# Optimization experiments

Measured on AMD Instinct MI355X. Metric: run time of the kernel, lower is better.

Reference implementation:

```python
import jax, jax.numpy as jnp
import numpy as np


def ste_sign(w):
    # straight-through binarization: forward sign(w), backward identity
    return w + jax.lax.stop_gradient(jnp.sign(w) - w)


def spike(x):
    # Heaviside spike with straight-through estimator
    return x + jax.lax.stop_gradient((x > 0).astype(x.dtype) - x)


def quantized_conv1d(x, w, b, stride, padding):
    # XNOR-Net style 1-bit weights: sign(w) * per-out-channel mean(|w|)
    alpha = jnp.mean(jnp.abs(w), axis=(1, 2), keepdims=True)  # (O,1,1)
    wq = ste_sign(w) * alpha
    y = jax.lax.conv_general_dilated(
        x, wq, window_strides=(stride,), padding=[(padding, padding)],
        dimension_numbers=('NCH', 'OIH', 'NCH'))
    return y + b[None, :, None]


def batchnorm(x, gamma, beta, eps=1e-5):
    # training-mode BN over (batch, length) per channel
    mu = jnp.mean(x, axis=(0, 2), keepdims=True)
    var = jnp.var(x, axis=(0, 2), keepdims=True)
    return (x - mu) * jax.lax.rsqrt(var + eps) * gamma[None, :, None] + beta[None, :, None]


def window_attn(sq, sk, sv, w):
    # spiking attention restricted to non-overlapping windows of size w
    B, L, C = sq.shape
    pad = (-L) % w
    p = lambda a: jnp.pad(a, ((0, 0), (0, pad), (0, 0)))  # zero-pad -> zero spikes
    q = p(sq).reshape(B, -1, w, C)
    k = p(sk).reshape(B, -1, w, C)
    v = p(sv).reshape(B, -1, w, C)
    attn = jnp.einsum('bnwc,bnuc->bnwu', q, k)           # (B, nW, w, w)
    out = jnp.einsum('bnwu,bnuc->bnwc', attn, v) / w
    return out.reshape(B, -1, C)[:, :L]


def global_attn(sq, K, V, g):
    # pool K,V down to g global tokens, then linear spiking attention
    B, L, C = K.shape
    chunk = -(-L // g)
    pad = chunk * g - L
    p = lambda a: jnp.pad(a, ((0, 0), (0, pad), (0, 0)))
    kp = p(K).reshape(B, g, chunk, C).mean(axis=2)       # (B, g, C)
    vp = p(V).reshape(B, g, chunk, C).mean(axis=2)
    skg, svg = spike(kp), spike(vp)
    kv = jnp.einsum('bgc,bgd->bcd', skg, svg)            # (B, C, C)
    return jnp.einsum('blc,bcd->bld', sq, kv) / g


def mssa(x, wq, wk, wv, wo, local_w=64, regional_w=256, global_pool=16):
    # x: (B, C, L) -> token-major (B, L, C)
    h = jnp.swapaxes(x, 1, 2)
    Q, K, V = h @ wq, h @ wk, h @ wv
    sq, sk, sv = spike(Q), spike(K), spike(V)
    out = (window_attn(sq, sk, sv, local_w)
           + window_attn(sq, sk, sv, regional_w)
           + global_attn(sq, K, V, global_pool)) / 3.0
    y = h + out @ wo  # residual
    return jnp.swapaxes(y, 1, 2)


def setup_inputs() -> dict:
    key = jax.random.key(0)
    ks = jax.random.split(key, 8)
    B, Cin, L, Cout = 32, 256, 5000, 128
    return {
        'x': jax.random.normal(ks[0], (B, Cin, L), jnp.float32),
        'conv_w': jax.random.normal(ks[1], (Cout, Cin, 9), jnp.float32) * 0.05,
        'conv_b': jnp.zeros((Cout,), jnp.float32),
        'gamma': jnp.ones((Cout,), jnp.float32),
        'beta': jnp.zeros((Cout,), jnp.float32),
        'wq': jax.random.normal(ks[2], (Cout, Cout), jnp.float32) * 0.09,
        'wk': jax.random.normal(ks[3], (Cout, Cout), jnp.float32) * 0.09,
        'wv': jax.random.normal(ks[4], (Cout, Cout), jnp.float32) * 0.09,
        'wo': jax.random.normal(ks[5], (Cout, Cout), jnp.float32) * 0.09,
    }


def reference(x, conv_w, conv_b, gamma, beta, wq, wk, wv, wo):
    y = quantized_conv1d(x, conv_w, conv_b, stride=2, padding=4)  # (B,128,2500)
    y = jax.nn.elu(batchnorm(y, gamma, beta))
    return mssa(y, wq, wk, wv, wo)                                # (B,128,2500)
```

## Files before the change

kernel.cpp:

```cpp
#include <hip/hip_runtime.h>

typedef __attribute__((ext_vector_type(8))) short bf16x8;
typedef __attribute__((ext_vector_type(4))) float f32x4;
typedef __attribute__((ext_vector_type(16))) float f32x16;
typedef __attribute__((ext_vector_type(4))) unsigned int u32x4;
typedef __attribute__((ext_vector_type(4))) int s32x4;
typedef unsigned short u16;
typedef unsigned int u32;

#define DI __device__ __forceinline__

constexpr int B_ = 32, CI = 256, LX = 5000, CO = 128, LO = 2500, KW = 9, LP = 2560;

DI float b2f(u16 u) { u32 x = ((u32)u) << 16; return __builtin_bit_cast(float, x); }
DI u16 f2b(float f) {
  u32 x = __builtin_bit_cast(u32, f);
  u32 r = (x + 0x7fffu + ((x >> 16) & 1u)) >> 16;
  return (u16)r;
}
DI float elu(float v) { return v > 0.f ? v : expm1f(v); }

__global__ __launch_bounds__(256) void k_prep_wq(const float* __restrict__ w, u16* __restrict__ wfmt,
                                                 float* __restrict__ alphaf) {
  int o = blockIdx.x;
  const float* wrow = w + o * CI * KW;
  float s = 0.f;
  for (int idx = threadIdx.x; idx < CI * KW; idx += 256) s += fabsf(wrow[idx]);
  __shared__ float red[256];
  red[threadIdx.x] = s;
  __syncthreads();
  for (int st = 128; st > 0; st >>= 1) {
    if (threadIdx.x < st) red[threadIdx.x] += red[threadIdx.x + st];
    __syncthreads();
  }
  if (threadIdx.x == 0) alphaf[o] = red[0] / (float)(CI * KW);
  for (int idx = threadIdx.x; idx < CI * KW; idx += 256) {
    int i = idx / KW, k = idx - i * KW;
    float v = wrow[idx];
    float sg = v > 0.f ? 1.f : (v < 0.f ? -1.f : 0.f);
    wfmt[(((k * 16) + (i >> 4)) * 128 + o) * 16 + (i & 15)] = f2b(sg);
  }
}

__global__ __launch_bounds__(256) void k_prep_wT(const float* __restrict__ wq, const float* __restrict__ wk,
                                                 const float* __restrict__ wv, const float* __restrict__ wo,
                                                 u16* __restrict__ wThi, u16* __restrict__ wTlo,
                                                 u16* __restrict__ wT3) {
  const float* src[4] = {wq, wk, wv, wo};
  int mat = blockIdx.x;
  const float* m = src[mat];
  u16* dh = wThi + mat * CO * CO;
  u16* dl = wTlo + mat * CO * CO;
  for (int idx = threadIdx.x; idx < CO * CO; idx += 256) {
    int nn = idx >> 7, kkn = idx & 127;
    float v = m[kkn * CO + nn];
    u16 hi = f2b(v);
    u16 lo = f2b(v - b2f(hi));
    dh[idx] = hi;
    dl[idx] = lo;
    if (mat < 3) {
      int nt = nn >> 4, n = nn & 15, ks = kkn >> 5, gj = kkn & 31;
      size_t base = (size_t)((mat * 4 + ks) * 8 + nt) * 1024 + n * 32 + gj;
      wT3[base] = hi;
      wT3[base + 512] = lo;
    }
  }
}

__global__ __launch_bounds__(512) void k_conv(const float* __restrict__ x, const u16* __restrict__ wfmt,
                                              const float* __restrict__ bias, const float* __restrict__ alphaf,
                                              float* __restrict__ y1) {
  const int ltile = blockIdx.x, b = blockIdx.y;
  const int l0 = ltile * 64;
  const int lin0 = 2 * l0 - 4;
  alignas(16) __shared__ u16 xsh[136 * 136];
  alignas(16) __shared__ u16 xsl[136 * 136];
  const int tid = threadIdx.x;
  const int wave = tid >> 6, lane = tid & 63;
  const int col = lane & 31, g = lane >> 5;
  const int o0 = (wave & 3) * 32;
  const int lw = (wave >> 2) * 32;
  f32x16 acch = {};
  f32x16 accl = {};
  for (int cpass = 0; cpass < 2; ++cpass) {
    const int c0 = cpass * 128;
    if (cpass) __syncthreads();
#pragma unroll
    for (int it = 0; it < 9; ++it) {
      int idx = tid + it * 512;
      if (idx < 4352) {
        int i = idx / 34, q = idx - i * 34;
        int lin = lin0 + q * 4;
        const float* xr = x + ((size_t)(b * CI + c0 + i)) * LX;
        float4 v4 = float4{0.f, 0.f, 0.f, 0.f};
        if (lin >= 0 && lin + 4 <= LX) v4 = *reinterpret_cast<const float4*>(xr + lin);
        const float* vp = reinterpret_cast<const float*>(&v4);
#pragma unroll
        for (int e = 0; e < 4; ++e) {
          int p = q * 4 + e;
          float v = vp[e];
          u16 hi = f2b(v);
          int colx = ((((i >> 3) ^ ((p >> 1) & 15)) & 15) << 3) | (i & 7);
          xsh[p * 136 + colx] = hi;
          xsl[p * 136 + colx] = f2b(v - b2f(hi));
        }
      }
    }
    __syncthreads();
    for (int kk = 0; kk < KW; ++kk) {
      bf16x8 af[8];
#pragma unroll
      for (int icg = 0; icg < 8; ++icg) {
        int chunk = kk * 16 + cpass * 8 + icg;
        af[icg] = *reinterpret_cast<const bf16x8*>(wfmt + ((size_t)chunk * 128 + o0 + col) * 16 + g * 8);
      }
      const int p = 2 * (lw + col) + kk;
      const int prow = p * 136;
      const int s = (p >> 1) & 15;
#pragma unroll
      for (int icg = 0; icg < 8; ++icg) {
        int blkoff = (((icg * 2 + g) ^ s) << 3);
        bf16x8 bh = *reinterpret_cast<const bf16x8*>(&xsh[prow + blkoff]);
        bf16x8 bl = *reinterpret_cast<const bf16x8*>(&xsl[prow + blkoff]);
        acch = __builtin_amdgcn_mfma_f32_32x32x16_bf16(af[icg], bh, acch, 0, 0, 0);
        accl = __builtin_amdgcn_mfma_f32_32x32x16_bf16(af[icg], bl, accl, 0, 0, 0);
      }
    }
  }
  const int l = l0 + lw + col;
  if (l < LO) {
#pragma unroll
    for (int r = 0; r < 16; ++r) {
      int o = o0 + (r & 3) + 8 * (r >> 2) + 4 * g;
      y1[(b * CO + o) * LO + l] = alphaf[o] * (acch[r] + accl[r]) + bias[o];
    }
  }
}

__global__ __launch_bounds__(256) void k_stats(const float* __restrict__ y1, float* __restrict__ ps,
                                               float* __restrict__ ps2) {
  int o = blockIdx.x, b = blockIdx.y;
  const float4* row = reinterpret_cast<const float4*>(y1 + (size_t)(b * CO + o) * LO);
  float s = 0.f, s2 = 0.f;
  for (int i = threadIdx.x; i < 625; i += 256) {
    float4 v = row[i];
    s += v.x + v.y + v.z + v.w;
    s2 += v.x * v.x + v.y * v.y + v.z * v.z + v.w * v.w;
  }
  __shared__ float r1[256], r2[256];
  r1[threadIdx.x] = s;
  r2[threadIdx.x] = s2;
  __syncthreads();
  for (int st = 128; st > 0; st >>= 1) {
    if (threadIdx.x < st) {
      r1[threadIdx.x] += r1[threadIdx.x + st];
      r2[threadIdx.x] += r2[threadIdx.x + st];
    }
    __syncthreads();
  }
  if (threadIdx.x == 0) {
    ps[b * CO + o] = r1[0];
    ps2[b * CO + o] = r2[0];
  }
}

__global__ void k_bnparams(const float* __restrict__ ps, const float* __restrict__ ps2,
                           const float* __restrict__ gamma, const float* __restrict__ beta,
                           float* __restrict__ bnsc, float* __restrict__ bnsh) {
  int o = threadIdx.x;
  float s = 0.f, s2 = 0.f;
  for (int b = 0; b < B_; ++b) {
    s += ps[b * CO + o];
    s2 += ps2[b * CO + o];
  }
  const float inv_n = 1.f / (float)(B_ * LO);
  float mu = s * inv_n;
  float var = s2 * inv_n - mu * mu;
  float sc = gamma[o] * rsqrtf(var + 1e-5f);
  bnsc[o] = sc;
  bnsh[o] = beta[o] - mu * sc;
}

__global__ __launch_bounds__(256) void k_qkv(const float* __restrict__ y1, const float* __restrict__ bnsc,
                                             const float* __restrict__ bnsh, const u16* __restrict__ wT3,
                                             signed char* __restrict__ sq8, signed char* __restrict__ sk8,
                                             u16* __restrict__ sv) {
  int tile = blockIdx.x, b = blockIdx.y;
  int tid = threadIdx.x, wave = tid >> 6, lane = tid & 63, n = lane & 15, g = lane >> 4;
  const int t0 = tile * 64;
  alignas(16) __shared__ u16 hshi[64 * 136];
  alignas(16) __shared__ u16 hslo[64 * 136];
  {
    int t = tid & 63;
    int l = t0 + t;
    if (l > LO - 1) l = LO - 1;
    for (int c = (tid >> 6); c < CO; c += 4) {
      float raw = y1[((size_t)b * CO + c) * LO + l];
      float e = elu(raw * bnsc[c] + bnsh[c]);
      u16 hi = f2b(e);
      hshi[t * 136 + c] = hi;
      hslo[t * 136 + c] = f2b(e - b2f(hi));
    }
  }
  __syncthreads();
  const u16* ah = &hshi[(wave * 16 + n) * 136];
  const u16* al = &hslo[(wave * 16 + n) * 136];
  for (int mat = 0; mat < 3; ++mat) {
    f32x4 acc[8] = {};
#pragma unroll
    for (int ks = 0; ks < 4; ++ks) {
      bf16x8 ahi = *reinterpret_cast<const bf16x8*>(ah + ks * 32 + g * 8);
      bf16x8 alo = *reinterpret_cast<const bf16x8*>(al + ks * 32 + g * 8);
      const u16* wbase = wT3 + (size_t)((mat * 4 + ks) * 8) * 1024 + n * 32 + g * 8;
#pragma unroll
      for (int nt = 0; nt < 8; ++nt) {
        bf16x8 bhi = *reinterpret_cast<const bf16x8*>(wbase + nt * 1024);
        bf16x8 blo = *reinterpret_cast<const bf16x8*>(wbase + nt * 1024 + 512);
        acc[nt] = __builtin_amdgcn_mfma_f32_16x16x32_bf16(ahi, bhi, acc[nt], 0, 0, 0);
        acc[nt] = __builtin_amdgcn_mfma_f32_16x16x32_bf16(ahi, blo, acc[nt], 0, 0, 0);
        acc[nt] = __builtin_amdgcn_mfma_f32_16x16x32_bf16(alo, bhi, acc[nt], 0, 0, 0);
        acc[nt] = __builtin_amdgcn_mfma_f32_16x16x32_bf16(alo, blo, acc[nt], 0, 0, 0);
      }
    }
#pragma unroll
    for (int nt = 0; nt < 8; ++nt) {
#pragma unroll
      for (int r = 0; r < 4; ++r) {
        int tok = t0 + wave * 16 + g * 4 + r;
        int c = nt * 16 + n;
        bool valid = tok < LO;
        float v = valid ? acc[nt][r] : 0.f;
        size_t oidx = ((size_t)b * LP + tok) * CO + c;
        if (mat == 2) {
          sv[oidx] = f2b(v > 0.f ? 1.f : 0.f);
        } else {
          signed char* so8 = (mat == 0) ? sq8 : sk8;
          so8[oidx] = v > 0.f ? 1 : 0;
        }
      }
    }
  }
}

__global__ __launch_bounds__(64) void k_poolh(const float* __restrict__ y1, const float* __restrict__ bnsc,
                                              const float* __restrict__ bnsh, float* __restrict__ hsum) {
  int c = blockIdx.x, b = blockIdx.y, lane = threadIdx.x;
  const float* row = y1 + ((size_t)b * CO + c) * LO;
  const float sc = bnsc[c], sh = bnsh[c];
  __shared__ float bins[16][64];
#pragma unroll
  for (int ch = 0; ch < 16; ++ch) bins[ch][lane] = 0.f;
  for (int j = lane; j < LO; j += 64) {
    float e = elu(row[j] * sc + sh);
    bins[j / 157][lane] += e;
  }
#pragma unroll
  for (int ch = 0; ch < 16; ++ch) {
    float v = bins[ch][lane];
    for (int off = 32; off > 0; off >>= 1) v += __shfl_down(v, off);
    if (lane == 0) hsum[(b * 16 + ch) * CO + c] = v;
  }
}

__global__ __launch_bounds__(256) void k_kv2(const float* __restrict__ hsum, const float* __restrict__ wk,
                                             const float* __restrict__ wv, signed char* __restrict__ kv8) {
  int b = blockIdx.x;
  __shared__ float hs[16 * 128], sks[16 * 128], svs[16 * 128];
  for (int i = threadIdx.x; i < 2048; i += 256) hs[i] = hsum[b * 2048 + i];
  __syncthreads();
  for (int idx = threadIdx.x; idx < 2048; idx += 256) {
    int gg = idx >> 7, c = idx & 127;
    float ak = 0.f, av = 0.f;
    for (int k = 0; k < 128; ++k) {
      float hv = hs[gg * 128 + k];
      ak += hv * wk[k * CO + c];
      av += hv * wv[k * CO + c];
    }
    sks[idx] = ak > 0.f ? 1.f : 0.f;
    svs[idx] = av > 0.f ? 1.f : 0.f;
  }
  __syncthreads();
  for (int idx = threadIdx.x; idx < CO * CO; idx += 256) {
    int d = idx >> 7, c = idx & 127;
    float s = 0.f;
#pragma unroll
    for (int gg = 0; gg < 16; ++gg) s += sks[gg * 128 + c] * svs[gg * 128 + d];
    kv8[b * CO * CO + idx] = (signed char)s;
  }
}

__global__ __launch_bounds__(512) void k_attn(const signed char* __restrict__ sq8,
                                              const signed char* __restrict__ sk8,
                                              const u16* __restrict__ sv, const signed char* __restrict__ kv8,
                                              const u16* __restrict__ woT, const float* __restrict__ y1,
                                              const float* __restrict__ bnsc, const float* __restrict__ bnsh,
                                              float* __restrict__ out) {
  const int win = blockIdx.x, b = blockIdx.y, qt = blockIdx.z;
  const int T0 = win * 256;
  alignas(16) __shared__ char smem[69632];
  u16* svT = reinterpret_cast<u16*>(smem);
  const int tid = threadIdx.x, wave = tid >> 6, lane = tid & 63, n = lane & 15, g = lane >> 4;
  for (int idx = tid; idx < 256 * 128; idx += 512) {
    int u = idx >> 7, c = idx & 127;
    svT[c * 264 + u] = sv[((size_t)b * LP + T0 + u) * CO + c];
  }
  __syncthreads();
  {
    const int qbase = wave * 32 + qt * 16;
    s32x4 bq8[2];
    const signed char* qrow = sq8 + ((size_t)b * LP + T0 + qbase + n) * CO;
    bq8[0] = *reinterpret_cast<const s32x4*>(qrow + g * 16);
    bq8[1] = *reinterpret_cast<const s32x4*>(qrow + 64 + g * 16);
    s32x4 pacc[16];
#pragma unroll
    for (int ut = 0; ut < 16; ++ut) pacc[ut] = s32x4{0, 0, 0, 0};
    for (int ut = 0; ut < 16; ++ut) {
      const signed char* krow = sk8 + ((size_t)b * LP + T0 + ut * 16 + n) * CO;
      s32x4 kf0 = *reinterpret_cast<const s32x4*>(krow + g * 16);
      s32x4 kf1 = *reinterpret_cast<const s32x4*>(krow + 64 + g * 16);
      pacc[ut] = __builtin_amdgcn_mfma_i32_16x16x64_i8(kf0, bq8[0], pacc[ut], 0, 0, 0);
      pacc[ut] = __builtin_amdgcn_mfma_i32_16x16x64_i8(kf1, bq8[1], pacc[ut], 0, 0, 0);
    }
    const int qblk = (qbase + n) >> 6;
    u32 packed[16][2];
#pragma unroll
    for (int ut = 0; ut < 16; ++ut) {
      u16 pk[4];
#pragma unroll
      for (int r = 0; r < 4; ++r) {
        int uloc = ut * 16 + g * 4 + r;
        float wgt = (1.f / 768.f) + (((uloc >> 6) == qblk) ? (1.f / 192.f) : 0.f);
        pk[r] = f2b((float)pacc[ut][r] * wgt);
      }
      packed[ut][0] = (u32)pk[0] | ((u32)pk[1] << 16);
      packed[ut][1] = (u32)pk[2] | ((u32)pk[3] << 16);
    }
    f32x4 acco[8];
#pragma unroll
    for (int ct = 0; ct < 8; ++ct) {
      s32x4 ag = {0, 0, 0, 0};
      const signed char* kvrow = kv8 + ((size_t)b * CO + ct * 16 + n) * CO;
      s32x4 k0 = *reinterpret_cast<const s32x4*>(kvrow + g * 16);
      s32x4 k1 = *reinterpret_cast<const s32x4*>(kvrow + 64 + g * 16);
      ag = __builtin_amdgcn_mfma_i32_16x16x64_i8(bq8[0], k0, ag, 0, 0, 0);
      ag = __builtin_amdgcn_mfma_i32_16x16x64_i8(bq8[1], k1, ag, 0, 0, 0);
#pragma unroll
      for (int r = 0; r < 4; ++r) acco[ct][r] = (float)ag[r] * (1.f / 48.f);
    }
    const int sl0 = n + 16 * ((g & 1) * 2);
    const int sl1 = sl0 + 16;
    const bool ghi = ((g >> 1) & 1) != 0;
#pragma unroll
    for (int us = 0; us < 8; ++us) {
      u32 a0e = (u32)__shfl((int)packed[us * 2][0], sl0, 64);
      u32 a0o = (u32)__shfl((int)packed[us * 2 + 1][0], sl0, 64);
      u32 a1e = (u32)__shfl((int)packed[us * 2][1], sl0, 64);
      u32 a1o = (u32)__shfl((int)packed[us * 2 + 1][1], sl0, 64);
      u32 a2e = (u32)__shfl((int)packed[us * 2][0], sl1, 64);
      u32 a2o = (u32)__shfl((int)packed[us * 2 + 1][0], sl1, 64);
      u32 a3e = (u32)__shfl((int)packed[us * 2][1], sl1, 64);
      u32 a3o = (u32)__shfl((int)packed[us * 2 + 1][1], sl1, 64);
      u32x4 paw = {ghi ? a0o : a0e, ghi ? a1o : a1e, ghi ? a2o : a2e, ghi ? a3o : a3e};
      bf16x8 pa = __builtin_bit_cast(bf16x8, paw);
#pragma unroll
      for (int ct = 0; ct < 8; ++ct) {
        bf16x8 bv = *reinterpret_cast<const bf16x8*>(&svT[(ct * 16 + n) * 264 + us * 32 + g * 8]);
        acco[ct] = __builtin_amdgcn_mfma_f32_16x16x32_bf16(pa, bv, acco[ct], 0, 0, 0);
      }
    }
    __syncthreads();
    u16* pw2 = reinterpret_cast<u16*>(smem) + wave * (16 * 136);
    float* sF = reinterpret_cast<float*>(smem + 34816) + wave * (64 * 17);
#pragma unroll
    for (int ct = 0; ct < 8; ++ct) {
#pragma unroll
      for (int r = 0; r < 4; ++r) {
        pw2[(g * 4 + r) * 136 + ct * 16 + n] = f2b(acco[ct][r]);
      }
    }
    for (int half = 0; half < 2; ++half) {
#pragma unroll
      for (int ot2 = 0; ot2 < 4; ++ot2) {
        int ot = half * 4 + ot2;
        f32x4 facc = {};
#pragma unroll
        for (int ks = 0; ks < 4; ++ks) {
          bf16x8 af = *reinterpret_cast<const bf16x8*>(&pw2[n * 136 + ks * 32 + g * 8]);
          bf16x8 bw = *reinterpret_cast<const bf16x8*>(woT + (ot * 16 + n) * CO + ks * 32 + g * 8);
          facc = __builtin_amdgcn_mfma_f32_16x16x32_bf16(af, bw, facc, 0, 0, 0);
        }
#pragma unroll
        for (int r = 0; r < 4; ++r) sF[(ot2 * 16 + n) * 17 + g * 4 + r] = facc[r];
      }
#pragma unroll
      for (int oo = 0; oo < 16; ++oo) {
        int olocal = oo * 4 + (lane >> 4);
        int o = half * 64 + olocal;
        int l = T0 + qbase + (lane & 15);
        float v = sF[olocal * 17 + (lane & 15)];
        if (l < LO) {
          size_t idx = ((size_t)b * CO + o) * LO + l;
          out[idx] = elu(y1[idx] * bnsc[o] + bnsh[o]) + v;
        }
      }
    }
  }
}

extern "C" void kernel_launch(void* const* d_in, const int* in_sizes, int n_in, void* d_out, int out_size,
                              void* d_ws, size_t ws_size, hipStream_t stream) {
  const float* x = (const float*)d_in[0];
  const float* conv_w = (const float*)d_in[1];
  const float* conv_b = (const float*)d_in[2];
  const float* gamma = (const float*)d_in[3];
  const float* beta = (const float*)d_in[4];
  const float* wq = (const float*)d_in[5];
  const float* wk = (const float*)d_in[6];
  const float* wv = (const float*)d_in[7];
  const float* wo = (const float*)d_in[8];
  (void)in_sizes; (void)n_in; (void)out_size; (void)ws_size;

  char* ws = (char*)d_ws;
  size_t off = 0;
  auto alloc = [&](size_t bytes) -> void* {
    void* p = ws + off;
    off += (bytes + 511) & ~(size_t)511;
    return p;
  };
  float* ps = (float*)alloc((size_t)B_ * CO * 4);
  float* ps2 = (float*)alloc((size_t)B_ * CO * 4);
  float* bnsc = (float*)alloc(CO * 4);
  float* bnsh = (float*)alloc(CO * 4);
  float* alphaf = (float*)alloc(CO * 4);
  float* hsum = (float*)alloc((size_t)B_ * 16 * CO * 4);
  signed char* kv8 = (signed char*)alloc((size_t)B_ * CO * CO);
  u16* wfmt = (u16*)alloc((size_t)CO * KW * CI * 2);
  u16* wThi = (u16*)alloc((size_t)4 * CO * CO * 2);
  u16* wTlo = (u16*)alloc((size_t)4 * CO * CO * 2);
  u16* wT3 = (u16*)alloc((size_t)3 * 4 * 8 * 1024 * 2);
  float* y1 = (float*)alloc((size_t)B_ * CO * LO * 4);
  signed char* sqb8 = (signed char*)alloc((size_t)B_ * LP * CO);
  signed char* skb8 = (signed char*)alloc((size_t)B_ * LP * CO);
  u16* svb = (u16*)alloc((size_t)B_ * LP * CO * 2);

  hipLaunchKernelGGL(k_prep_wq, dim3(CO), dim3(256), 0, stream, conv_w, wfmt, alphaf);
  hipLaunchKernelGGL(k_prep_wT, dim3(4), dim3(256), 0, stream, wq, wk, wv, wo, wThi, wTlo, wT3);
  hipLaunchKernelGGL(k_conv, dim3(40, B_), dim3(512), 0, stream, x, wfmt, conv_b, alphaf, y1);
  hipLaunchKernelGGL(k_stats, dim3(CO, B_), dim3(256), 0, stream, y1, ps, ps2);
  hipLaunchKernelGGL(k_bnparams, dim3(1), dim3(CO), 0, stream, ps, ps2, gamma, beta, bnsc, bnsh);
  hipLaunchKernelGGL(k_qkv, dim3(40, B_), dim3(256), 0, stream, y1, bnsc, bnsh, wT3, sqb8, skb8, svb);
  hipLaunchKernelGGL(k_poolh, dim3(CO, B_), dim3(64), 0, stream, y1, bnsc, bnsh, hsum);
  hipLaunchKernelGGL(k_kv2, dim3(B_), dim3(256), 0, stream, hsum, wk, wv, kv8);
  hipLaunchKernelGGL(k_attn, dim3(10, B_, 2), dim3(512), 0, stream, sqb8, skb8, svb, kv8, wThi + 3 * CO * CO,
                     y1, bnsc, bnsh, (float*)d_out);
}
```

Measured before the change: 469.2 us.

## Halve conv L-tile to 32 with 256-thread blocks and merge prep kernels

Shrinks the conv tile from 64 to 32 output positions, so each block has 4 waves and about half the shared memory. The grid doubles to 80x32 blocks, which should raise occupancy and block count on the GPU. In exchange, the input halo (8 extra rows of 72) is reloaded relative to useful work, and weight fragments are reused across fewer columns. The two weight-prep kernels are also merged into a single launch to save one launch.

```diff
diff --git a/kernel.cpp b/kernel.cpp
--- a/kernel.cpp
+++ b/kernel.cpp
@@ -20,66 +20,65 @@
 }
 DI float elu(float v) { return v > 0.f ? v : expm1f(v); }
 
-__global__ __launch_bounds__(256) void k_prep_wq(const float* __restrict__ w, u16* __restrict__ wfmt,
-                                                 float* __restrict__ alphaf) {
-  int o = blockIdx.x;
-  const float* wrow = w + o * CI * KW;
-  float s = 0.f;
-  for (int idx = threadIdx.x; idx < CI * KW; idx += 256) s += fabsf(wrow[idx]);
-  __shared__ float red[256];
-  red[threadIdx.x] = s;
-  __syncthreads();
-  for (int st = 128; st > 0; st >>= 1) {
-    if (threadIdx.x < st) red[threadIdx.x] += red[threadIdx.x + st];
+__global__ __launch_bounds__(256) void k_prep(const float* __restrict__ w, const float* __restrict__ wq,
+                                              const float* __restrict__ wk, const float* __restrict__ wv,
+                                              const float* __restrict__ wo, u16* __restrict__ wfmt,
+                                              float* __restrict__ alphaf, u16* __restrict__ wThi,
+                                              u16* __restrict__ wTlo, u16* __restrict__ wT3) {
+  if (blockIdx.x < 128) {
+    int o = blockIdx.x;
+    const float* wrow = w + o * CI * KW;
+    float s = 0.f;
+    for (int idx = threadIdx.x; idx < CI * KW; idx += 256) s += fabsf(wrow[idx]);
+    __shared__ float red[256];
+    red[threadIdx.x] = s;
     __syncthreads();
-  }
-  if (threadIdx.x == 0) alphaf[o] = red[0] / (float)(CI * KW);
-  for (int idx = threadIdx.x; idx < CI * KW; idx += 256) {
-    int i = idx / KW, k = idx - i * KW;
-    float v = wrow[idx];
-    float sg = v > 0.f ? 1.f : (v < 0.f ? -1.f : 0.f);
-    wfmt[(((k * 16) + (i >> 4)) * 128 + o) * 16 + (i & 15)] = f2b(sg);
-  }
-}
-
-__global__ __launch_bounds__(256) void k_prep_wT(const float* __restrict__ wq, const float* __restrict__ wk,
-                                                 const float* __restrict__ wv, const float* __restrict__ wo,
-                                                 u16* __restrict__ wThi, u16* __restrict__ wTlo,
-                                                 u16* __restrict__ wT3) {
-  const float* src[4] = {wq, wk, wv, wo};
-  int mat = blockIdx.x;
-  const float* m = src[mat];
-  u16* dh = wThi + mat * CO * CO;
-  u16* dl = wTlo + mat * CO * CO;
-  for (int idx = threadIdx.x; idx < CO * CO; idx += 256) {
-    int nn = idx >> 7, kkn = idx & 127;
-    float v = m[kkn * CO + nn];
-    u16 hi = f2b(v);
-    u16 lo = f2b(v - b2f(hi));
-    dh[idx] = hi;
-    dl[idx] = lo;
-    if (mat < 3) {
-      int nt = nn >> 4, n = nn & 15, ks = kkn >> 5, gj = kkn & 31;
-      size_t base = (size_t)((mat * 4 + ks) * 8 + nt) * 1024 + n * 32 + gj;
-      wT3[base] = hi;
-      wT3[base + 512] = lo;
-    }
-  }
-}
-
-__global__ __launch_bounds__(512) void k_conv(const float* __restrict__ x, const u16* __restrict__ wfmt,
+    for (int st = 128; st > 0; st >>= 1) {
+      if (threadIdx.x < st) red[threadIdx.x] += red[threadIdx.x + st];
+      __syncthreads();
+    }
+    if (threadIdx.x == 0) alphaf[o] = red[0] / (float)(CI * KW);
+    for (int idx = threadIdx.x; idx < CI * KW; idx += 256) {
+      int i = idx / KW, k = idx - i * KW;
+      float v = wrow[idx];
+      float sg = v > 0.f ? 1.f : (v < 0.f ? -1.f : 0.f);
+      wfmt[(((k * 16) + (i >> 4)) * 128 + o) * 16 + (i & 15)] = f2b(sg);
+    }
+  } else {
+    const float* src[4] = {wq, wk, wv, wo};
+    int mat = blockIdx.x - 128;
+    const float* m = src[mat];
+    u16* dh = wThi + mat * CO * CO;
+    u16* dl = wTlo + mat * CO * CO;
+    for (int idx = threadIdx.x; idx < CO * CO; idx += 256) {
+      int nn = idx >> 7, kkn = idx & 127;
+      float v = m[kkn * CO + nn];
+      u16 hi = f2b(v);
+      u16 lo = f2b(v - b2f(hi));
+      dh[idx] = hi;
+      dl[idx] = lo;
+      if (mat < 3) {
+        int nt = nn >> 4, n = nn & 15, ks = kkn >> 5, gj = kkn & 31;
+        size_t base = (size_t)((mat * 4 + ks) * 8 + nt) * 1024 + n * 32 + gj;
+        wT3[base] = hi;
+        wT3[base + 512] = lo;
+      }
+    }
+  }
+}
+
+__global__ __launch_bounds__(256) void k_conv(const float* __restrict__ x, const u16* __restrict__ wfmt,
                                               const float* __restrict__ bias, const float* __restrict__ alphaf,
                                               float* __restrict__ y1) {
   const int ltile = blockIdx.x, b = blockIdx.y;
-  const int l0 = ltile * 64;
+  const int l0 = ltile * 32;
   const int lin0 = 2 * l0 - 4;
-  alignas(16) __shared__ u16 xsh[136 * 136];
-  alignas(16) __shared__ u16 xsl[136 * 136];
+  alignas(16) __shared__ u16 xsh[72 * 136];
+  alignas(16) __shared__ u16 xsl[72 * 136];
   const int tid = threadIdx.x;
   const int wave = tid >> 6, lane = tid & 63;
   const int col = lane & 31, g = lane >> 5;
-  const int o0 = (wave & 3) * 32;
-  const int lw = (wave >> 2) * 32;
+  const int o0 = wave * 32;
   f32x16 acch = {};
   f32x16 accl = {};
   for (int cpass = 0; cpass < 2; ++cpass) {
@@ -87,23 +86,21 @@
     if (cpass) __syncthreads();
 #pragma unroll
     for (int it = 0; it < 9; ++it) {
-      int idx = tid + it * 512;
-      if (idx < 4352) {
-        int i = idx / 34, q = idx - i * 34;
-        int lin = lin0 + q * 4;
-        const float* xr = x + ((size_t)(b * CI + c0 + i)) * LX;
-        float4 v4 = float4{0.f, 0.f, 0.f, 0.f};
-        if (lin >= 0 && lin + 4 <= LX) v4 = *reinterpret_cast<const float4*>(xr + lin);
-        const float* vp = reinterpret_cast<const float*>(&v4);
-#pragma unroll
-        for (int e = 0; e < 4; ++e) {
-          int p = q * 4 + e;
-          float v = vp[e];
-          u16 hi = f2b(v);
-          int colx = ((((i >> 3) ^ ((p >> 1) & 15)) & 15) << 3) | (i & 7);
-          xsh[p * 136 + colx] = hi;
-          xsl[p * 136 + colx] = f2b(v - b2f(hi));
-        }
+      int idx = tid + it * 256;
+      int i = idx / 18, q = idx - i * 18;
+      int lin = lin0 + q * 4;
+      const float* xr = x + ((size_t)(b * CI + c0 + i)) * LX;
+      float4 v4 = float4{0.f, 0.f, 0.f, 0.f};
+      if (lin >= 0 && lin + 4 <= LX) v4 = *reinterpret_cast<const float4*>(xr + lin);
+      const float* vp = reinterpret_cast<const float*>(&v4);
+#pragma unroll
+      for (int e = 0; e < 4; ++e) {
+        int p = q * 4 + e;
+        float v = vp[e];
+        u16 hi = f2b(v);
+        int colx = ((((i >> 3) ^ ((p >> 1) & 15)) & 15) << 3) | (i & 7);
+        xsh[p * 136 + colx] = hi;
+        xsl[p * 136 + colx] = f2b(v - b2f(hi));
       }
     }
     __syncthreads();
@@ -114,7 +111,7 @@
         int chunk = kk * 16 + cpass * 8 + icg;
         af[icg] = *reinterpret_cast<const bf16x8*>(wfmt + ((size_t)chunk * 128 + o0 + col) * 16 + g * 8);
       }
-      const int p = 2 * (lw + col) + kk;
+      const int p = 2 * col + kk;
       const int prow = p * 136;
       const int s = (p >> 1) & 15;
 #pragma unroll
@@ -127,7 +124,7 @@
       }
     }
   }
-  const int l = l0 + lw + col;
+  const int l = l0 + col;
   if (l < LO) {
 #pragma unroll
     for (int r = 0; r < 16; ++r) {
@@ -386,7 +383,7 @@
 #pragma unroll
         for (int ks = 0; ks < 4; ++ks) {
           bf16x8 af = *reinterpret_cast<const bf16x8*>(&pw2[n * 136 + ks * 32 + g * 8]);
-          bf16x8 bw = *reinterpret_cast<const bf16x8*>(woT + (ot * 16 + n) * CO + ks * 32 + g * 8);
+          bf16x8 bw = *reinterpret_cast<const bf16x8*>(&woT[(ot * 16 + n) * CO + ks * 32 + g * 8]);
           facc = __builtin_amdgcn_mfma_f32_16x16x32_bf16(af, bw, facc, 0, 0, 0);
         }
 #pragma unroll
@@ -443,9 +440,9 @@
   signed char* skb8 = (signed char*)alloc((size_t)B_ * LP * CO);
   u16* svb = (u16*)alloc((size_t)B_ * LP * CO * 2);
 
-  hipLaunchKernelGGL(k_prep_wq, dim3(CO), dim3(256), 0, stream, conv_w, wfmt, alphaf);
-  hipLaunchKernelGGL(k_prep_wT, dim3(4), dim3(256), 0, stream, wq, wk, wv, wo, wThi, wTlo, wT3);
-  hipLaunchKernelGGL(k_conv, dim3(40, B_), dim3(512), 0, stream, x, wfmt, conv_b, alphaf, y1);
+  hipLaunchKernelGGL(k_prep, dim3(132), dim3(256), 0, stream, conv_w, wq, wk, wv, wo, wfmt, alphaf, wThi,
+                     wTlo, wT3);
+  hipLaunchKernelGGL(k_conv, dim3(80, B_), dim3(256), 0, stream, x, wfmt, conv_b, alphaf, y1);
   hipLaunchKernelGGL(k_stats, dim3(CO, B_), dim3(256), 0, stream, y1, ps, ps2);
   hipLaunchKernelGGL(k_bnparams, dim3(1), dim3(CO), 0, stream, ps, ps2, gamma, beta, bnsc, bnsh);
   hipLaunchKernelGGL(k_qkv, dim3(40, B_), dim3(256), 0, stream, y1, bnsc, bnsh, wT3, sqb8, skb8, svb);
```

New measurement: 427.1 us. 1.1x faster.
